# Performance work log

Measured on AMD Instinct MI355X. Metric: run time of the kernel, lower is better.

The kernel has to match this reference:

```python
import jax, jax.numpy as jnp
import numpy as np

N_NODES = 50000
N_EDGES = 500000
F_IN = 16
F_OUT = 16
F_EDGE = 16
HIDDEN = 64


def setup_inputs() -> dict:
    key = jax.random.key(0)
    ks = jax.random.split(key, 9)
    return {
        "x": jax.random.normal(ks[0], (N_NODES, F_IN), dtype=jnp.float32),
        "edge_feat": jax.random.normal(ks[1], (N_EDGES, F_EDGE), dtype=jnp.float32),
        "src": jax.random.randint(ks[2], (N_EDGES,), 0, N_NODES, dtype=jnp.int32),
        "dst": jax.random.randint(ks[3], (N_EDGES,), 0, N_NODES, dtype=jnp.int32),
        "W1": jax.random.normal(ks[4], (F_EDGE, HIDDEN), dtype=jnp.float32) * 0.1,
        "b1": jax.random.normal(ks[5], (HIDDEN,), dtype=jnp.float32) * 0.1,
        "W2": jax.random.normal(ks[6], (HIDDEN, F_IN * F_OUT), dtype=jnp.float32) * 0.1,
        "b2": jax.random.normal(ks[7], (F_IN * F_OUT,), dtype=jnp.float32) * 0.1,
        "bias": jax.random.normal(ks[8], (F_OUT,), dtype=jnp.float32) * 0.1,
    }


def reference(x, edge_feat, src, dst, W1, b1, W2, b2, bias):
    # WeightNet: per-edge MLP producing a [F_IN, F_OUT] weight matrix per edge
    h = jax.nn.relu(edge_feat @ W1 + b1)                 # [E, HIDDEN]
    W = (h @ W2 + b2).reshape(-1, F_IN, F_OUT)           # [E, F_IN, F_OUT]
    # message: bmm(src_h[E,1,in], W[E,in,out]) -> [E, F_OUT]
    msg = jnp.einsum('ei,eio->eo', x[src], W)
    # scatter-mean reduce over destination nodes
    msum = jax.ops.segment_sum(msg, dst, num_segments=N_NODES)
    cnt = jax.ops.segment_sum(jnp.ones((msg.shape[0],), dtype=msg.dtype), dst,
                              num_segments=N_NODES)
    mean = msum / jnp.maximum(cnt, 1.0)[:, None]
    # DGL update_all only updates nodes that receive messages; zero in-degree
    # nodes keep their input 'h' (valid since F_IN == F_OUT)
    out = jnp.where((cnt > 0)[:, None], mean, x)
    return out + bias[None, :]                           # [N, F_OUT]
```

## Files before the change

kernel.cpp:

```cpp
#include <hip/hip_runtime.h>

#define NN 50000
#define NE 500000
#define FIN 16
#define FOUT 16
#define HID 64
#define TROW 1040
#define NPW 16

typedef unsigned int  uint;
typedef unsigned short ushort;

__device__ __forceinline__ ushort f2bf(float f) {
    uint u = __float_as_uint(f);
    u += 0x7fffu + ((u >> 16) & 1u);
    return (ushort)(u >> 16);
}
__device__ __forceinline__ float bflo(uint u) { return __uint_as_float(u << 16); }
__device__ __forceinline__ float bfhi(uint u) { return __uint_as_float(u & 0xffff0000u); }


__global__ __launch_bounds__(256) void w2r_prep(
    const float* __restrict__ W2, const float* __restrict__ b2,
    float* __restrict__ W2R)
{
    const int t = blockIdx.x * blockDim.x + threadIdx.x;
    if (t >= 65 * 256) return;
    const int j = t >> 8;
    const int col = t & 255;
    const int i = col >> 4, o = col & 15;
    const float v = (j < 64) ? W2[j * 256 + col] : b2[col];
    W2R[j * 256 + o * 16 + i] = v;
}

__global__ __launch_bounds__(256) void count_both(
    const int* __restrict__ src, const int* __restrict__ dst,
    int* __restrict__ deg_s, int* __restrict__ pos_s, int* __restrict__ deg_d)
{
    const int e = blockIdx.x * blockDim.x + threadIdx.x;
    if (e >= NE) return;
    pos_s[e] = atomicAdd(deg_s + src[e], 1);
    atomicAdd(deg_d + dst[e], 1);
}

__global__ __launch_bounds__(1024) void dgc_scan2(
    const int* __restrict__ degA, int* __restrict__ offA,
    const int* __restrict__ degB, int* __restrict__ offB)
{
    const int* __restrict__ deg = blockIdx.x ? degB : degA;
    int* __restrict__ offs      = blockIdx.x ? offB : offA;
    __shared__ int wsum[16];
    const int tid = threadIdx.x;
    const int lane = tid & 63;
    const int wid = tid >> 6;
    int carry = 0;
    for (int base = 0; base < NN; base += 1024) {
        const int idx = base + tid;
        const int v = (idx < NN) ? deg[idx] : 0;
        int s = v;
        #pragma unroll
        for (int d = 1; d < 64; d <<= 1) {
            int t = __shfl_up(s, d, 64);
            if (lane >= d) s += t;
        }
        if (lane == 63) wsum[wid] = s;
        __syncthreads();
        if (wid == 0 && lane < 16) {
            int w = wsum[lane];
            #pragma unroll
            for (int d = 1; d < 16; d <<= 1) {
                int t = __shfl_up(w, d, 64);
                if (lane >= d) w += t;
            }
            wsum[lane] = w;
        }
        __syncthreads();
        const int wpre = (wid == 0) ? 0 : wsum[wid - 1];
        if (idx < NN) offs[idx] = carry + wpre + (s - v);
        carry += wsum[15];
        __syncthreads();
    }
    if (tid == 0) offs[NN] = carry;
}

__global__ __launch_bounds__(256) void scatter_src(
    const int* __restrict__ src, const int* __restrict__ pos_s,
    const int* __restrict__ offs_s, int* __restrict__ eidx_s)
{
    const int e = blockIdx.x * blockDim.x + threadIdx.x;
    if (e >= NE) return;
    eidx_s[offs_s[src[e]] + pos_s[e]] = e;
}

__global__ __launch_bounds__(256) void tprep4(
    const float* __restrict__ x, const float* __restrict__ W2R,
    ushort* __restrict__ T)
{
    __shared__ ushort w2b[65 * 288];
    const int tid = threadIdx.x;
    for (int g = tid; g < 65 * 256; g += 256) {
        const int j = g >> 8, col = g & 255;
        const int oo = col >> 4, ii = col & 15;
        w2b[j * 288 + oo * 18 + ii] = f2bf(W2R[g]);
    }
    __syncthreads();

    const int w = tid >> 6, lane = tid & 63;
    const int j4 = lane >> 4, o = lane & 15;
    const int nbase = (blockIdx.x * 4 + w) * NPW;

    for (int t = 0; t < NPW; ++t) {
        const int n = nbase + t;
        if (n >= NN) break;

        float xr[16];
        {
            const float4* p = reinterpret_cast<const float4*>(x) + (size_t)n * 4;
            float4 a = p[0], b = p[1], c = p[2], d = p[3];
            xr[0]=a.x; xr[1]=a.y; xr[2]=a.z;  xr[3]=a.w;
            xr[4]=b.x; xr[5]=b.y; xr[6]=b.z;  xr[7]=b.w;
            xr[8]=c.x; xr[9]=c.y; xr[10]=c.z; xr[11]=c.w;
            xr[12]=d.x; xr[13]=d.y; xr[14]=d.z; xr[15]=d.w;
        }

        ushort* tw = T + (size_t)n * TROW;
        #pragma unroll
        for (int k = 0; k < 17; ++k) {
            const int j = j4 + (k << 2);
            if (j < 65) {
                const uint* wu = reinterpret_cast<const uint*>(w2b + j * 288 + o * 18);
                float s = 0.f;
                #pragma unroll
                for (int q = 0; q < 8; ++q) {
                    const uint u = wu[q];
                    s = fmaf(xr[2 * q],     bflo(u), s);
                    s = fmaf(xr[2 * q + 1], bfhi(u), s);
                }
                tw[j * 16 + o] = f2bf(s);
            }
        }
    }
}

__global__ __launch_bounds__(256) void edge_msg2(
    const int* __restrict__ eidx_s, const int* __restrict__ src,
    const int* __restrict__ dst, const float* __restrict__ ef,
    const float* __restrict__ W1, const float* __restrict__ b1,
    const ushort* __restrict__ T, const int* __restrict__ offs_d,
    int* __restrict__ cur_d, float* __restrict__ msgbuf)
{
    const int k = blockIdx.x * blockDim.x + threadIdx.x;
    if (k >= NE) return;
    const int e = eidx_s[k];
    const int s = src[e];

    float efv[16];
    {
        const float4* p = reinterpret_cast<const float4*>(ef) + (size_t)e * 4;
        float4 a = p[0], b = p[1], c = p[2], d = p[3];
        efv[0]=a.x; efv[1]=a.y; efv[2]=a.z;  efv[3]=a.w;
        efv[4]=b.x; efv[5]=b.y; efv[6]=b.z;  efv[7]=b.w;
        efv[8]=c.x; efv[9]=c.y; efv[10]=c.z; efv[11]=c.w;
        efv[12]=d.x; efv[13]=d.y; efv[14]=d.z; efv[15]=d.w;
    }

    const ushort* tr = T + (size_t)s * TROW;
    float m[16];
    {
        uint4 a = *reinterpret_cast<const uint4*>(tr + 1024);
        uint4 b = *reinterpret_cast<const uint4*>(tr + 1032);
        m[0]=bflo(a.x);  m[1]=bfhi(a.x);  m[2]=bflo(a.y);  m[3]=bfhi(a.y);
        m[4]=bflo(a.z);  m[5]=bfhi(a.z);  m[6]=bflo(a.w);  m[7]=bfhi(a.w);
        m[8]=bflo(b.x);  m[9]=bfhi(b.x);  m[10]=bflo(b.y); m[11]=bfhi(b.y);
        m[12]=bflo(b.z); m[13]=bfhi(b.z); m[14]=bflo(b.w); m[15]=bfhi(b.w);
    }

    for (int j = 0; j < HID; ++j) {
        float hj = b1[j];
        #pragma unroll
        for (int i = 0; i < 16; ++i)
            hj = fmaf(efv[i], W1[i * HID + j], hj);
        hj = fmaxf(hj, 0.f);

        uint4 a = *reinterpret_cast<const uint4*>(tr + j * 16);
        uint4 b = *reinterpret_cast<const uint4*>(tr + j * 16 + 8);
        m[0]  = fmaf(hj, bflo(a.x), m[0]);  m[1]  = fmaf(hj, bfhi(a.x), m[1]);
        m[2]  = fmaf(hj, bflo(a.y), m[2]);  m[3]  = fmaf(hj, bfhi(a.y), m[3]);
        m[4]  = fmaf(hj, bflo(a.z), m[4]);  m[5]  = fmaf(hj, bfhi(a.z), m[5]);
        m[6]  = fmaf(hj, bflo(a.w), m[6]);  m[7]  = fmaf(hj, bfhi(a.w), m[7]);
        m[8]  = fmaf(hj, bflo(b.x), m[8]);  m[9]  = fmaf(hj, bfhi(b.x), m[9]);
        m[10] = fmaf(hj, bflo(b.y), m[10]); m[11] = fmaf(hj, bfhi(b.y), m[11]);
        m[12] = fmaf(hj, bflo(b.z), m[12]); m[13] = fmaf(hj, bfhi(b.z), m[13]);
        m[14] = fmaf(hj, bflo(b.w), m[14]); m[15] = fmaf(hj, bfhi(b.w), m[15]);
    }

    const int d = dst[e];
    const int slot = offs_d[d] + atomicAdd(cur_d + d, 1);
    float4* mr = reinterpret_cast<float4*>(msgbuf + (size_t)slot * 16);
    mr[0] = make_float4(m[0], m[1], m[2], m[3]);
    mr[1] = make_float4(m[4], m[5], m[6], m[7]);
    mr[2] = make_float4(m[8], m[9], m[10], m[11]);
    mr[3] = make_float4(m[12], m[13], m[14], m[15]);
}

__global__ __launch_bounds__(256) void gather_mean2(
    const float* __restrict__ msgbuf, const int* __restrict__ offs_d,
    const float* __restrict__ x, const float* __restrict__ bias,
    float* __restrict__ out)
{
    const int t = blockIdx.x * blockDim.x + threadIdx.x;
    if (t >= NN * FOUT) return;
    const int n = t >> 4;
    const int o = t & 15;
    const int beg = offs_d[n], end = offs_d[n + 1];
    float s = 0.f;
    for (int k = beg; k < end; ++k)
        s += msgbuf[(size_t)k * 16 + o];
    const int d = end - beg;
    const float v = (d > 0) ? (s / (float)d) : x[t];
    out[t] = v + bias[o];
}

__global__ __launch_bounds__(1024) void dgc_scan(
    const int* __restrict__ deg, int* __restrict__ offs, int n)
{
    __shared__ int wsum[16];
    const int tid = threadIdx.x;
    const int lane = tid & 63;
    const int wid = tid >> 6;
    int carry = 0;
    for (int base = 0; base < n; base += 1024) {
        const int idx = base + tid;
        const int v = (idx < n) ? deg[idx] : 0;
        int s = v;
        #pragma unroll
        for (int d = 1; d < 64; d <<= 1) {
            int t = __shfl_up(s, d, 64);
            if (lane >= d) s += t;
        }
        if (lane == 63) wsum[wid] = s;
        __syncthreads();
        if (wid == 0 && lane < 16) {
            int w = wsum[lane];
            #pragma unroll
            for (int d = 1; d < 16; d <<= 1) {
                int t = __shfl_up(w, d, 64);
                if (lane >= d) w += t;
            }
            wsum[lane] = w;
        }
        __syncthreads();
        const int wpre = (wid == 0) ? 0 : wsum[wid - 1];
        if (idx < n) offs[idx] = carry + wpre + (s - v);
        carry += wsum[15];
        __syncthreads();
    }
    if (tid == 0) offs[n] = carry;
}

__global__ __launch_bounds__(256) void dgc_edge_csr(
    const float* __restrict__ x, const float* __restrict__ ef,
    const int* __restrict__ src, const int* __restrict__ dst,
    const float* __restrict__ W1, const float* __restrict__ b1,
    const float* __restrict__ W2, const float* __restrict__ b2,
    float* __restrict__ msg, int* __restrict__ pos, int* __restrict__ deg)
{
    const int e = blockIdx.x * blockDim.x + threadIdx.x;
    if (e >= NE) return;
    float efv[16];
    {
        const float4* p = reinterpret_cast<const float4*>(ef) + (size_t)e * 4;
        float4 a = p[0], b = p[1], c = p[2], d = p[3];
        efv[0]=a.x; efv[1]=a.y; efv[2]=a.z;  efv[3]=a.w;
        efv[4]=b.x; efv[5]=b.y; efv[6]=b.z;  efv[7]=b.w;
        efv[8]=c.x; efv[9]=c.y; efv[10]=c.z; efv[11]=c.w;
        efv[12]=d.x; efv[13]=d.y; efv[14]=d.z; efv[15]=d.w;
    }
    const int s = src[e];
    float xs[16];
    {
        const float4* p = reinterpret_cast<const float4*>(x) + (size_t)s * 4;
        float4 a = p[0], b = p[1], c = p[2], d = p[3];
        xs[0]=a.x; xs[1]=a.y; xs[2]=a.z;  xs[3]=a.w;
        xs[4]=b.x; xs[5]=b.y; xs[6]=b.z;  xs[7]=b.w;
        xs[8]=c.x; xs[9]=c.y; xs[10]=c.z; xs[11]=c.w;
        xs[12]=d.x; xs[13]=d.y; xs[14]=d.z; xs[15]=d.w;
    }
    float m[16];
    #pragma unroll
    for (int o = 0; o < 16; ++o) m[o] = 0.f;
    #pragma unroll
    for (int i = 0; i < 16; ++i) {
        const float xi = xs[i];
        #pragma unroll
        for (int o = 0; o < 16; ++o) m[o] = fmaf(xi, b2[i * 16 + o], m[o]);
    }
    for (int j = 0; j < HID; ++j) {
        float hj = b1[j];
        #pragma unroll
        for (int i = 0; i < 16; ++i) hj = fmaf(efv[i], W1[i * HID + j], hj);
        hj = fmaxf(hj, 0.f);
        const float* __restrict__ w2r = W2 + (size_t)j * 256;
        float t[16];
        #pragma unroll
        for (int o = 0; o < 16; ++o) t[o] = 0.f;
        #pragma unroll
        for (int i = 0; i < 16; ++i) {
            const float xi = xs[i];
            #pragma unroll
            for (int o = 0; o < 16; ++o) t[o] = fmaf(xi, w2r[i * 16 + o], t[o]);
        }
        #pragma unroll
        for (int o = 0; o < 16; ++o) m[o] = fmaf(hj, t[o], m[o]);
    }
    float4* mr = reinterpret_cast<float4*>(msg + (size_t)e * 16);
    mr[0] = make_float4(m[0], m[1], m[2], m[3]);
    mr[1] = make_float4(m[4], m[5], m[6], m[7]);
    mr[2] = make_float4(m[8], m[9], m[10], m[11]);
    mr[3] = make_float4(m[12], m[13], m[14], m[15]);
    pos[e] = atomicAdd(deg + dst[e], 1);
}

__global__ __launch_bounds__(256) void dgc_scatter(
    const int* __restrict__ dst, const int* __restrict__ pos,
    const int* __restrict__ offs, int* __restrict__ eidx)
{
    const int e = blockIdx.x * blockDim.x + threadIdx.x;
    if (e >= NE) return;
    eidx[offs[dst[e]] + pos[e]] = e;
}

__global__ __launch_bounds__(256) void dgc_gather(
    const float* __restrict__ msg, const int* __restrict__ offs,
    const int* __restrict__ eidx, const float* __restrict__ x,
    const float* __restrict__ bias, float* __restrict__ out)
{
    const int t = blockIdx.x * blockDim.x + threadIdx.x;
    if (t >= NN * FOUT) return;
    const int n = t >> 4;
    const int o = t & 15;
    const int beg = offs[n], end = offs[n + 1];
    float s = 0.f;
    for (int k = beg; k < end; ++k)
        s += msg[(size_t)eidx[k] * 16 + o];
    const int d = end - beg;
    const float v = (d > 0) ? (s / (float)d) : x[t];
    out[t] = v + bias[o];
}

extern "C" void kernel_launch(void* const* d_in, const int* in_sizes, int n_in,
                              void* d_out, int out_size, void* d_ws, size_t ws_size,
                              hipStream_t stream) {
    const float* x    = (const float*)d_in[0];
    const float* ef   = (const float*)d_in[1];
    const int*   src  = (const int*)d_in[2];
    const int*   dst  = (const int*)d_in[3];
    const float* W1   = (const float*)d_in[4];
    const float* b1   = (const float*)d_in[5];
    const float* W2   = (const float*)d_in[6];
    const float* b2   = (const float*)d_in[7];
    const float* bias = (const float*)d_in[8];
    float* out = (float*)d_out;

    ushort* T      = (ushort*)d_ws;
    float*  msgbuf = (float*)(T + (size_t)NN * TROW);
    float*  W2R    = msgbuf + (size_t)NE * 16;
    int*    deg_s  = (int*)(W2R + 65 * 256);
    int*    deg_d  = deg_s + NN;
    int*    cur_d  = deg_d + NN;
    int*    offs_s = cur_d + NN;
    int*    offs_d = offs_s + NN + 1;
    int*    pos_s  = offs_d + NN + 1;
    int*    eidx_s = pos_s + NE;
    const size_t needed =
        (size_t)NN * TROW * 2 +
        ((size_t)NE * 16 + 65 * 256) * 4 +
        ((size_t)3 * NN + 2 * (NN + 1) + (size_t)2 * NE) * 4;

    if (ws_size >= needed) {
        hipMemsetAsync(deg_s, 0, (size_t)3 * NN * sizeof(int), stream);
        w2r_prep<<<(65 * 256 + 255) / 256, 256, 0, stream>>>(W2, b2, W2R);
        count_both<<<(NE + 255) / 256, 256, 0, stream>>>(src, dst, deg_s, pos_s, deg_d);
        dgc_scan2<<<2, 1024, 0, stream>>>(deg_s, offs_s, deg_d, offs_d);
        scatter_src<<<(NE + 255) / 256, 256, 0, stream>>>(src, pos_s, offs_s, eidx_s);
        tprep4<<<(NN + 4 * NPW - 1) / (4 * NPW), 256, 0, stream>>>(x, W2R, T);
        edge_msg2<<<(NE + 255) / 256, 256, 0, stream>>>(
            eidx_s, src, dst, ef, W1, b1, T, offs_d, cur_d, msgbuf);
        gather_mean2<<<(NN * FOUT + 255) / 256, 256, 0, stream>>>(
            msgbuf, offs_d, x, bias, out);
    } else {
        float* msg  = (float*)d_ws;
        int*   deg  = (int*)(msg + (size_t)NE * 16);
        int*   offs = deg + NN;
        int*   pos  = offs + NN + 1;
        int*   eidx = pos + NE;
        hipMemsetAsync(deg, 0, (size_t)NN * sizeof(int), stream);
        dgc_edge_csr<<<(NE + 255) / 256, 256, 0, stream>>>(
            x, ef, src, dst, W1, b1, W2, b2, msg, pos, deg);
        dgc_scan<<<1, 1024, 0, stream>>>(deg, offs, NN);
        dgc_scatter<<<(NE + 255) / 256, 256, 0, stream>>>(dst, pos, offs, eidx);
        dgc_gather<<<(NN * FOUT + 255) / 256, 256, 0, stream>>>(
            msg, offs, eidx, x, bias, out);
    }
}
```

Before: 259.9 us.

## Keep W2 slices in registers for T prep and process two edges per thread

The per-node T-table kernel now keeps each thread's W2R slices in fp32 registers and uses a grid-stride loop over nodes, one node per block iteration. This replaces the shared-memory bf16 staging of the weights and the per-block conversion cost. The edge message kernel now handles two consecutive sorted edges per thread, sharing W1 loads across both and exposing more independent loads and FMAs. The cost is higher register pressure, which may reduce occupancy. Skipping the bf16 rounding of the weights also changes numerics slightly.

```diff
diff --git a/kernel.cpp b/kernel.cpp
--- a/kernel.cpp
+++ b/kernel.cpp
@@ -6,7 +6,6 @@
 #define FOUT 16
 #define HID 64
 #define TROW 1040
-#define NPW 16
 
 typedef unsigned int  uint;
 typedef unsigned short ushort;
@@ -92,27 +91,37 @@
     eidx_s[offs_s[src[e]] + pos_s[e]] = e;
 }
 
-__global__ __launch_bounds__(256) void tprep4(
+__global__ __launch_bounds__(256) void tprep5(
     const float* __restrict__ x, const float* __restrict__ W2R,
     ushort* __restrict__ T)
 {
-    __shared__ ushort w2b[65 * 288];
     const int tid = threadIdx.x;
-    for (int g = tid; g < 65 * 256; g += 256) {
-        const int j = g >> 8, col = g & 255;
-        const int oo = col >> 4, ii = col & 15;
-        w2b[j * 288 + oo * 18 + ii] = f2bf(W2R[g]);
-    }
-    __syncthreads();
-
-    const int w = tid >> 6, lane = tid & 63;
-    const int j4 = lane >> 4, o = lane & 15;
-    const int nbase = (blockIdx.x * 4 + w) * NPW;
-
-    for (int t = 0; t < NPW; ++t) {
-        const int n = nbase + t;
-        if (n >= NN) break;
-
+    const int jt = tid >> 4, o = tid & 15;
+
+    float w0[16], w1[16], w2[16], w3[16];
+    {
+        const float4* p0 = reinterpret_cast<const float4*>(W2R + (jt     ) * 256 + o * 16);
+        const float4* p1 = reinterpret_cast<const float4*>(W2R + (jt + 16) * 256 + o * 16);
+        const float4* p2 = reinterpret_cast<const float4*>(W2R + (jt + 32) * 256 + o * 16);
+        const float4* p3 = reinterpret_cast<const float4*>(W2R + (jt + 48) * 256 + o * 16);
+        #pragma unroll
+        for (int q = 0; q < 4; ++q) {
+            float4 a = p0[q]; w0[4*q]=a.x; w0[4*q+1]=a.y; w0[4*q+2]=a.z; w0[4*q+3]=a.w;
+            float4 b = p1[q]; w1[4*q]=b.x; w1[4*q+1]=b.y; w1[4*q+2]=b.z; w1[4*q+3]=b.w;
+            float4 c = p2[q]; w2[4*q]=c.x; w2[4*q+1]=c.y; w2[4*q+2]=c.z; w2[4*q+3]=c.w;
+            float4 d = p3[q]; w3[4*q]=d.x; w3[4*q+1]=d.y; w3[4*q+2]=d.z; w3[4*q+3]=d.w;
+        }
+    }
+    float wb[16];
+    if (jt == 0) {
+        const float4* pb = reinterpret_cast<const float4*>(W2R + 64 * 256 + o * 16);
+        #pragma unroll
+        for (int q = 0; q < 4; ++q) {
+            float4 a = pb[q]; wb[4*q]=a.x; wb[4*q+1]=a.y; wb[4*q+2]=a.z; wb[4*q+3]=a.w;
+        }
+    }
+
+    for (int n = blockIdx.x; n < NN; n += gridDim.x) {
         float xr[16];
         {
             const float4* p = reinterpret_cast<const float4*>(x) + (size_t)n * 4;
@@ -122,85 +131,134 @@
             xr[8]=c.x; xr[9]=c.y; xr[10]=c.z; xr[11]=c.w;
             xr[12]=d.x; xr[13]=d.y; xr[14]=d.z; xr[15]=d.w;
         }
-
         ushort* tw = T + (size_t)n * TROW;
-        #pragma unroll
-        for (int k = 0; k < 17; ++k) {
-            const int j = j4 + (k << 2);
-            if (j < 65) {
-                const uint* wu = reinterpret_cast<const uint*>(w2b + j * 288 + o * 18);
-                float s = 0.f;
-                #pragma unroll
-                for (int q = 0; q < 8; ++q) {
-                    const uint u = wu[q];
-                    s = fmaf(xr[2 * q],     bflo(u), s);
-                    s = fmaf(xr[2 * q + 1], bfhi(u), s);
-                }
-                tw[j * 16 + o] = f2bf(s);
-            }
-        }
-    }
-}
-
-__global__ __launch_bounds__(256) void edge_msg2(
+
+        float s0 = xr[0]*w0[0], s1 = xr[0]*w1[0], s2 = xr[0]*w2[0], s3 = xr[0]*w3[0];
+        #pragma unroll
+        for (int i = 1; i < 16; ++i) {
+            s0 = fmaf(xr[i], w0[i], s0);
+            s1 = fmaf(xr[i], w1[i], s1);
+            s2 = fmaf(xr[i], w2[i], s2);
+            s3 = fmaf(xr[i], w3[i], s3);
+        }
+        tw[tid]       = f2bf(s0);
+        tw[tid + 256] = f2bf(s1);
+        tw[tid + 512] = f2bf(s2);
+        tw[tid + 768] = f2bf(s3);
+        if (jt == 0) {
+            float sb = xr[0]*wb[0];
+            #pragma unroll
+            for (int i = 1; i < 16; ++i) sb = fmaf(xr[i], wb[i], sb);
+            tw[1024 + o] = f2bf(sb);
+        }
+    }
+}
+
+__global__ __launch_bounds__(256) void edge_msg3(
     const int* __restrict__ eidx_s, const int* __restrict__ src,
     const int* __restrict__ dst, const float* __restrict__ ef,
     const float* __restrict__ W1, const float* __restrict__ b1,
     const ushort* __restrict__ T, const int* __restrict__ offs_d,
     int* __restrict__ cur_d, float* __restrict__ msgbuf)
 {
-    const int k = blockIdx.x * blockDim.x + threadIdx.x;
-    if (k >= NE) return;
-    const int e = eidx_s[k];
-    const int s = src[e];
-
-    float efv[16];
-    {
-        const float4* p = reinterpret_cast<const float4*>(ef) + (size_t)e * 4;
+    const int k0 = (blockIdx.x * blockDim.x + threadIdx.x) * 2;
+    if (k0 >= NE) return;
+    const bool two = (k0 + 1 < NE);
+    const int k1 = two ? (k0 + 1) : k0;
+
+    const int e0 = eidx_s[k0], e1 = eidx_s[k1];
+    const int s0 = src[e0],    s1 = src[e1];
+
+    float ea[16], eb[16];
+    {
+        const float4* p = reinterpret_cast<const float4*>(ef) + (size_t)e0 * 4;
         float4 a = p[0], b = p[1], c = p[2], d = p[3];
-        efv[0]=a.x; efv[1]=a.y; efv[2]=a.z;  efv[3]=a.w;
-        efv[4]=b.x; efv[5]=b.y; efv[6]=b.z;  efv[7]=b.w;
-        efv[8]=c.x; efv[9]=c.y; efv[10]=c.z; efv[11]=c.w;
-        efv[12]=d.x; efv[13]=d.y; efv[14]=d.z; efv[15]=d.w;
-    }
-
-    const ushort* tr = T + (size_t)s * TROW;
-    float m[16];
-    {
-        uint4 a = *reinterpret_cast<const uint4*>(tr + 1024);
-        uint4 b = *reinterpret_cast<const uint4*>(tr + 1032);
-        m[0]=bflo(a.x);  m[1]=bfhi(a.x);  m[2]=bflo(a.y);  m[3]=bfhi(a.y);
-        m[4]=bflo(a.z);  m[5]=bfhi(a.z);  m[6]=bflo(a.w);  m[7]=bfhi(a.w);
-        m[8]=bflo(b.x);  m[9]=bfhi(b.x);  m[10]=bflo(b.y); m[11]=bfhi(b.y);
-        m[12]=bflo(b.z); m[13]=bfhi(b.z); m[14]=bflo(b.w); m[15]=bfhi(b.w);
+        ea[0]=a.x; ea[1]=a.y; ea[2]=a.z;  ea[3]=a.w;
+        ea[4]=b.x; ea[5]=b.y; ea[6]=b.z;  ea[7]=b.w;
+        ea[8]=c.x; ea[9]=c.y; ea[10]=c.z; ea[11]=c.w;
+        ea[12]=d.x; ea[13]=d.y; ea[14]=d.z; ea[15]=d.w;
+    }
+    {
+        const float4* p = reinterpret_cast<const float4*>(ef) + (size_t)e1 * 4;
+        float4 a = p[0], b = p[1], c = p[2], d = p[3];
+        eb[0]=a.x; eb[1]=a.y; eb[2]=a.z;  eb[3]=a.w;
+        eb[4]=b.x; eb[5]=b.y; eb[6]=b.z;  eb[7]=b.w;
+        eb[8]=c.x; eb[9]=c.y; eb[10]=c.z; eb[11]=c.w;
+        eb[12]=d.x; eb[13]=d.y; eb[14]=d.z; eb[15]=d.w;
+    }
+
+    const ushort* tr0 = T + (size_t)s0 * TROW;
+    const ushort* tr1 = T + (size_t)s1 * TROW;
+
+    float m0[16], m1[16];
+    {
+        uint4 a = *reinterpret_cast<const uint4*>(tr0 + 1024);
+        uint4 b = *reinterpret_cast<const uint4*>(tr0 + 1032);
+        m0[0]=bflo(a.x);  m0[1]=bfhi(a.x);  m0[2]=bflo(a.y);  m0[3]=bfhi(a.y);
+        m0[4]=bflo(a.z);  m0[5]=bfhi(a.z);  m0[6]=bflo(a.w);  m0[7]=bfhi(a.w);
+        m0[8]=bflo(b.x);  m0[9]=bfhi(b.x);  m0[10]=bflo(b.y); m0[11]=bfhi(b.y);
+        m0[12]=bflo(b.z); m0[13]=bfhi(b.z); m0[14]=bflo(b.w); m0[15]=bfhi(b.w);
+    }
+    {
+        uint4 a = *reinterpret_cast<const uint4*>(tr1 + 1024);
+        uint4 b = *reinterpret_cast<const uint4*>(tr1 + 1032);
+        m1[0]=bflo(a.x);  m1[1]=bfhi(a.x);  m1[2]=bflo(a.y);  m1[3]=bfhi(a.y);
+        m1[4]=bflo(a.z);  m1[5]=bfhi(a.z);  m1[6]=bflo(a.w);  m1[7]=bfhi(a.w);
+        m1[8]=bflo(b.x);  m1[9]=bfhi(b.x);  m1[10]=bflo(b.y); m1[11]=bfhi(b.y);
+        m1[12]=bflo(b.z); m1[13]=bfhi(b.z); m1[14]=bflo(b.w); m1[15]=bfhi(b.w);
     }
 
     for (int j = 0; j < HID; ++j) {
-        float hj = b1[j];
-        #pragma unroll
-        for (int i = 0; i < 16; ++i)
-            hj = fmaf(efv[i], W1[i * HID + j], hj);
-        hj = fmaxf(hj, 0.f);
-
-        uint4 a = *reinterpret_cast<const uint4*>(tr + j * 16);
-        uint4 b = *reinterpret_cast<const uint4*>(tr + j * 16 + 8);
-        m[0]  = fmaf(hj, bflo(a.x), m[0]);  m[1]  = fmaf(hj, bfhi(a.x), m[1]);
-        m[2]  = fmaf(hj, bflo(a.y), m[2]);  m[3]  = fmaf(hj, bfhi(a.y), m[3]);
-        m[4]  = fmaf(hj, bflo(a.z), m[4]);  m[5]  = fmaf(hj, bfhi(a.z), m[5]);
-        m[6]  = fmaf(hj, bflo(a.w), m[6]);  m[7]  = fmaf(hj, bfhi(a.w), m[7]);
-        m[8]  = fmaf(hj, bflo(b.x), m[8]);  m[9]  = fmaf(hj, bfhi(b.x), m[9]);
-        m[10] = fmaf(hj, bflo(b.y), m[10]); m[11] = fmaf(hj, bfhi(b.y), m[11]);
-        m[12] = fmaf(hj, bflo(b.z), m[12]); m[13] = fmaf(hj, bfhi(b.z), m[13]);
-        m[14] = fmaf(hj, bflo(b.w), m[14]); m[15] = fmaf(hj, bfhi(b.w), m[15]);
-    }
-
-    const int d = dst[e];
-    const int slot = offs_d[d] + atomicAdd(cur_d + d, 1);
-    float4* mr = reinterpret_cast<float4*>(msgbuf + (size_t)slot * 16);
-    mr[0] = make_float4(m[0], m[1], m[2], m[3]);
-    mr[1] = make_float4(m[4], m[5], m[6], m[7]);
-    mr[2] = make_float4(m[8], m[9], m[10], m[11]);
-    mr[3] = make_float4(m[12], m[13], m[14], m[15]);
+        float h0 = b1[j], h1 = h0;
+        #pragma unroll
+        for (int i = 0; i < 16; ++i) {
+            const float w = W1[i * HID + j];
+            h0 = fmaf(ea[i], w, h0);
+            h1 = fmaf(eb[i], w, h1);
+        }
+        h0 = fmaxf(h0, 0.f);
+        h1 = fmaxf(h1, 0.f);
+
+        uint4 a0 = *reinterpret_cast<const uint4*>(tr0 + j * 16);
+        uint4 b0 = *reinterpret_cast<const uint4*>(tr0 + j * 16 + 8);
+        uint4 a1 = *reinterpret_cast<const uint4*>(tr1 + j * 16);
+        uint4 b1v = *reinterpret_cast<const uint4*>(tr1 + j * 16 + 8);
+        m0[0]  = fmaf(h0, bflo(a0.x), m0[0]);  m0[1]  = fmaf(h0, bfhi(a0.x), m0[1]);
+        m0[2]  = fmaf(h0, bflo(a0.y), m0[2]);  m0[3]  = fmaf(h0, bfhi(a0.y), m0[3]);
+        m0[4]  = fmaf(h0, bflo(a0.z), m0[4]);  m0[5]  = fmaf(h0, bfhi(a0.z), m0[5]);
+        m0[6]  = fmaf(h0, bflo(a0.w), m0[6]);  m0[7]  = fmaf(h0, bfhi(a0.w), m0[7]);
+        m0[8]  = fmaf(h0, bflo(b0.x), m0[8]);  m0[9]  = fmaf(h0, bfhi(b0.x), m0[9]);
+        m0[10] = fmaf(h0, bflo(b0.y), m0[10]); m0[11] = fmaf(h0, bfhi(b0.y), m0[11]);
+        m0[12] = fmaf(h0, bflo(b0.z), m0[12]); m0[13] = fmaf(h0, bfhi(b0.z), m0[13]);
+        m0[14] = fmaf(h0, bflo(b0.w), m0[14]); m0[15] = fmaf(h0, bfhi(b0.w), m0[15]);
+        m1[0]  = fmaf(h1, bflo(a1.x), m1[0]);  m1[1]  = fmaf(h1, bfhi(a1.x), m1[1]);
+        m1[2]  = fmaf(h1, bflo(a1.y), m1[2]);  m1[3]  = fmaf(h1, bfhi(a1.y), m1[3]);
+        m1[4]  = fmaf(h1, bflo(a1.z), m1[4]);  m1[5]  = fmaf(h1, bfhi(a1.z), m1[5]);
+        m1[6]  = fmaf(h1, bflo(a1.w), m1[6]);  m1[7]  = fmaf(h1, bfhi(a1.w), m1[7]);
+        m1[8]  = fmaf(h1, bflo(b1v.x), m1[8]);  m1[9]  = fmaf(h1, bfhi(b1v.x), m1[9]);
+        m1[10] = fmaf(h1, bflo(b1v.y), m1[10]); m1[11] = fmaf(h1, bfhi(b1v.y), m1[11]);
+        m1[12] = fmaf(h1, bflo(b1v.z), m1[12]); m1[13] = fmaf(h1, bfhi(b1v.z), m1[13]);
+        m1[14] = fmaf(h1, bflo(b1v.w), m1[14]); m1[15] = fmaf(h1, bfhi(b1v.w), m1[15]);
+    }
+
+    {
+        const int d = dst[e0];
+        const int slot = offs_d[d] + atomicAdd(cur_d + d, 1);
+        float4* mr = reinterpret_cast<float4*>(msgbuf + (size_t)slot * 16);
+        mr[0] = make_float4(m0[0], m0[1], m0[2], m0[3]);
+        mr[1] = make_float4(m0[4], m0[5], m0[6], m0[7]);
+        mr[2] = make_float4(m0[8], m0[9], m0[10], m0[11]);
+        mr[3] = make_float4(m0[12], m0[13], m0[14], m0[15]);
+    }
+    if (two) {
+        const int d = dst[e1];
+        const int slot = offs_d[d] + atomicAdd(cur_d + d, 1);
+        float4* mr = reinterpret_cast<float4*>(msgbuf + (size_t)slot * 16);
+        mr[0] = make_float4(m1[0], m1[1], m1[2], m1[3]);
+        mr[1] = make_float4(m1[4], m1[5], m1[6], m1[7]);
+        mr[2] = make_float4(m1[8], m1[9], m1[10], m1[11]);
+        mr[3] = make_float4(m1[12], m1[13], m1[14], m1[15]);
+    }
 }
 
 __global__ __launch_bounds__(256) void gather_mean2(
@@ -383,8 +441,8 @@
         count_both<<<(NE + 255) / 256, 256, 0, stream>>>(src, dst, deg_s, pos_s, deg_d);
         dgc_scan2<<<2, 1024, 0, stream>>>(deg_s, offs_s, deg_d, offs_d);
         scatter_src<<<(NE + 255) / 256, 256, 0, stream>>>(src, pos_s, offs_s, eidx_s);
-        tprep4<<<(NN + 4 * NPW - 1) / (4 * NPW), 256, 0, stream>>>(x, W2R, T);
-        edge_msg2<<<(NE + 255) / 256, 256, 0, stream>>>(
+        tprep5<<<2048, 256, 0, stream>>>(x, W2R, T);
+        edge_msg3<<<(NE / 2 + 255) / 256, 256, 0, stream>>>(
             eidx_s, src, dst, ef, W1, b1, T, offs_d, cur_d, msgbuf);
         gather_mean2<<<(NN * FOUT + 255) / 256, 256, 0, stream>>>(
             msgbuf, offs_d, x, bias, out);
```

Result: faster. 233.2 us (-10.3%).

## Register-resident W2 in T precompute, transposed W1 chunks, atomic-free dst slots

Applied to the files above, without the earlier changes.

The per-node T precompute now keeps its W2 slice in fp32 registers and runs a grid-stride loop with one node per block iteration, instead of staging bf16 weights in shared memory. The edge kernel reads a transposed W1 and computes hidden units in chunks of 16, giving a contiguous weight access pattern and more instruction-level parallelism. The destination slot comes from a position recorded during the count pass, so the per-edge atomic on a cursor array is gone, at the cost of an extra NE-sized int buffer. Register pressure rises in both kernels.

```diff
diff --git a/kernel.cpp b/kernel.cpp
--- a/kernel.cpp
+++ b/kernel.cpp
@@ -6,7 +6,6 @@
 #define FOUT 16
 #define HID 64
 #define TROW 1040
-#define NPW 16
 
 typedef unsigned int  uint;
 typedef unsigned short ushort;
@@ -22,9 +21,14 @@
 
 __global__ __launch_bounds__(256) void w2r_prep(
     const float* __restrict__ W2, const float* __restrict__ b2,
-    float* __restrict__ W2R)
+    const float* __restrict__ W1, float* __restrict__ W2R,
+    float* __restrict__ W1T)
 {
     const int t = blockIdx.x * blockDim.x + threadIdx.x;
+    if (t < 64 * 16) {
+        const int j = t >> 4, i = t & 15;
+        W1T[t] = W1[i * HID + j];
+    }
     if (t >= 65 * 256) return;
     const int j = t >> 8;
     const int col = t & 255;
@@ -35,12 +39,13 @@
 
 __global__ __launch_bounds__(256) void count_both(
     const int* __restrict__ src, const int* __restrict__ dst,
-    int* __restrict__ deg_s, int* __restrict__ pos_s, int* __restrict__ deg_d)
+    int* __restrict__ deg_s, int* __restrict__ pos_s,
+    int* __restrict__ deg_d, int* __restrict__ pos_d)
 {
     const int e = blockIdx.x * blockDim.x + threadIdx.x;
     if (e >= NE) return;
     pos_s[e] = atomicAdd(deg_s + src[e], 1);
-    atomicAdd(deg_d + dst[e], 1);
+    pos_d[e] = atomicAdd(deg_d + dst[e], 1);
 }
 
 __global__ __launch_bounds__(1024) void dgc_scan2(
@@ -92,27 +97,37 @@
     eidx_s[offs_s[src[e]] + pos_s[e]] = e;
 }
 
-__global__ __launch_bounds__(256) void tprep4(
+__global__ __launch_bounds__(256) void tprep5(
     const float* __restrict__ x, const float* __restrict__ W2R,
     ushort* __restrict__ T)
 {
-    __shared__ ushort w2b[65 * 288];
     const int tid = threadIdx.x;
-    for (int g = tid; g < 65 * 256; g += 256) {
-        const int j = g >> 8, col = g & 255;
-        const int oo = col >> 4, ii = col & 15;
-        w2b[j * 288 + oo * 18 + ii] = f2bf(W2R[g]);
-    }
-    __syncthreads();
-
-    const int w = tid >> 6, lane = tid & 63;
-    const int j4 = lane >> 4, o = lane & 15;
-    const int nbase = (blockIdx.x * 4 + w) * NPW;
-
-    for (int t = 0; t < NPW; ++t) {
-        const int n = nbase + t;
-        if (n >= NN) break;
-
+    const int jt = tid >> 4, o = tid & 15;
+
+    float w0[16], w1[16], w2[16], w3[16];
+    {
+        const float4* p0 = reinterpret_cast<const float4*>(W2R + (jt     ) * 256 + o * 16);
+        const float4* p1 = reinterpret_cast<const float4*>(W2R + (jt + 16) * 256 + o * 16);
+        const float4* p2 = reinterpret_cast<const float4*>(W2R + (jt + 32) * 256 + o * 16);
+        const float4* p3 = reinterpret_cast<const float4*>(W2R + (jt + 48) * 256 + o * 16);
+        #pragma unroll
+        for (int q = 0; q < 4; ++q) {
+            float4 a = p0[q]; w0[4*q]=a.x; w0[4*q+1]=a.y; w0[4*q+2]=a.z; w0[4*q+3]=a.w;
+            float4 b = p1[q]; w1[4*q]=b.x; w1[4*q+1]=b.y; w1[4*q+2]=b.z; w1[4*q+3]=b.w;
+            float4 c = p2[q]; w2[4*q]=c.x; w2[4*q+1]=c.y; w2[4*q+2]=c.z; w2[4*q+3]=c.w;
+            float4 d = p3[q]; w3[4*q]=d.x; w3[4*q+1]=d.y; w3[4*q+2]=d.z; w3[4*q+3]=d.w;
+        }
+    }
+    float wb[16];
+    if (jt == 0) {
+        const float4* pb = reinterpret_cast<const float4*>(W2R + 64 * 256 + o * 16);
+        #pragma unroll
+        for (int q = 0; q < 4; ++q) {
+            float4 a = pb[q]; wb[4*q]=a.x; wb[4*q+1]=a.y; wb[4*q+2]=a.z; wb[4*q+3]=a.w;
+        }
+    }
+
+    for (int n = blockIdx.x; n < NN; n += gridDim.x) {
         float xr[16];
         {
             const float4* p = reinterpret_cast<const float4*>(x) + (size_t)n * 4;
@@ -122,32 +137,35 @@
             xr[8]=c.x; xr[9]=c.y; xr[10]=c.z; xr[11]=c.w;
             xr[12]=d.x; xr[13]=d.y; xr[14]=d.z; xr[15]=d.w;
         }
-
         ushort* tw = T + (size_t)n * TROW;
-        #pragma unroll
-        for (int k = 0; k < 17; ++k) {
-            const int j = j4 + (k << 2);
-            if (j < 65) {
-                const uint* wu = reinterpret_cast<const uint*>(w2b + j * 288 + o * 18);
-                float s = 0.f;
-                #pragma unroll
-                for (int q = 0; q < 8; ++q) {
-                    const uint u = wu[q];
-                    s = fmaf(xr[2 * q],     bflo(u), s);
-                    s = fmaf(xr[2 * q + 1], bfhi(u), s);
-                }
-                tw[j * 16 + o] = f2bf(s);
-            }
-        }
-    }
-}
-
-__global__ __launch_bounds__(256) void edge_msg2(
+
+        float s0 = xr[0]*w0[0], s1 = xr[0]*w1[0], s2 = xr[0]*w2[0], s3 = xr[0]*w3[0];
+        #pragma unroll
+        for (int i = 1; i < 16; ++i) {
+            s0 = fmaf(xr[i], w0[i], s0);
+            s1 = fmaf(xr[i], w1[i], s1);
+            s2 = fmaf(xr[i], w2[i], s2);
+            s3 = fmaf(xr[i], w3[i], s3);
+        }
+        tw[tid]       = f2bf(s0);
+        tw[tid + 256] = f2bf(s1);
+        tw[tid + 512] = f2bf(s2);
+        tw[tid + 768] = f2bf(s3);
+        if (jt == 0) {
+            float sb = xr[0]*wb[0];
+            #pragma unroll
+            for (int i = 1; i < 16; ++i) sb = fmaf(xr[i], wb[i], sb);
+            tw[1024 + o] = f2bf(sb);
+        }
+    }
+}
+
+__global__ __launch_bounds__(256) void edge_msg4(
     const int* __restrict__ eidx_s, const int* __restrict__ src,
     const int* __restrict__ dst, const float* __restrict__ ef,
-    const float* __restrict__ W1, const float* __restrict__ b1,
+    const float* __restrict__ W1T, const float* __restrict__ b1,
     const ushort* __restrict__ T, const int* __restrict__ offs_d,
-    int* __restrict__ cur_d, float* __restrict__ msgbuf)
+    const int* __restrict__ pos_d, float* __restrict__ msgbuf)
 {
     const int k = blockIdx.x * blockDim.x + threadIdx.x;
     if (k >= NE) return;
@@ -175,27 +193,39 @@
         m[12]=bflo(b.z); m[13]=bfhi(b.z); m[14]=bflo(b.w); m[15]=bfhi(b.w);
     }
 
-    for (int j = 0; j < HID; ++j) {
-        float hj = b1[j];
-        #pragma unroll
-        for (int i = 0; i < 16; ++i)
-            hj = fmaf(efv[i], W1[i * HID + j], hj);
-        hj = fmaxf(hj, 0.f);
-
-        uint4 a = *reinterpret_cast<const uint4*>(tr + j * 16);
-        uint4 b = *reinterpret_cast<const uint4*>(tr + j * 16 + 8);
-        m[0]  = fmaf(hj, bflo(a.x), m[0]);  m[1]  = fmaf(hj, bfhi(a.x), m[1]);
-        m[2]  = fmaf(hj, bflo(a.y), m[2]);  m[3]  = fmaf(hj, bfhi(a.y), m[3]);
-        m[4]  = fmaf(hj, bflo(a.z), m[4]);  m[5]  = fmaf(hj, bfhi(a.z), m[5]);
-        m[6]  = fmaf(hj, bflo(a.w), m[6]);  m[7]  = fmaf(hj, bfhi(a.w), m[7]);
-        m[8]  = fmaf(hj, bflo(b.x), m[8]);  m[9]  = fmaf(hj, bfhi(b.x), m[9]);
-        m[10] = fmaf(hj, bflo(b.y), m[10]); m[11] = fmaf(hj, bfhi(b.y), m[11]);
-        m[12] = fmaf(hj, bflo(b.z), m[12]); m[13] = fmaf(hj, bfhi(b.z), m[13]);
-        m[14] = fmaf(hj, bflo(b.w), m[14]); m[15] = fmaf(hj, bfhi(b.w), m[15]);
+    for (int jc = 0; jc < 4; ++jc) {
+        const float*  wc = W1T + jc * 256;
+        const float*  bc = b1 + jc * 16;
+        const ushort* tc = tr + jc * 256;
+
+        float hh[16];
+        #pragma unroll
+        for (int jj = 0; jj < 16; ++jj) {
+            float hj = bc[jj];
+            #pragma unroll
+            for (int i = 0; i < 16; ++i)
+                hj = fmaf(efv[i], wc[jj * 16 + i], hj);
+            hh[jj] = fmaxf(hj, 0.f);
+        }
+
+        #pragma unroll
+        for (int jj = 0; jj < 16; ++jj) {
+            const float h = hh[jj];
+            uint4 a = *reinterpret_cast<const uint4*>(tc + jj * 16);
+            uint4 b = *reinterpret_cast<const uint4*>(tc + jj * 16 + 8);
+            m[0]  = fmaf(h, bflo(a.x), m[0]);  m[1]  = fmaf(h, bfhi(a.x), m[1]);
+            m[2]  = fmaf(h, bflo(a.y), m[2]);  m[3]  = fmaf(h, bfhi(a.y), m[3]);
+            m[4]  = fmaf(h, bflo(a.z), m[4]);  m[5]  = fmaf(h, bfhi(a.z), m[5]);
+            m[6]  = fmaf(h, bflo(a.w), m[6]);  m[7]  = fmaf(h, bfhi(a.w), m[7]);
+            m[8]  = fmaf(h, bflo(b.x), m[8]);  m[9]  = fmaf(h, bfhi(b.x), m[9]);
+            m[10] = fmaf(h, bflo(b.y), m[10]); m[11] = fmaf(h, bfhi(b.y), m[11]);
+            m[12] = fmaf(h, bflo(b.z), m[12]); m[13] = fmaf(h, bfhi(b.z), m[13]);
+            m[14] = fmaf(h, bflo(b.w), m[14]); m[15] = fmaf(h, bfhi(b.w), m[15]);
+        }
     }
 
     const int d = dst[e];
-    const int slot = offs_d[d] + atomicAdd(cur_d + d, 1);
+    const int slot = offs_d[d] + pos_d[e];
     float4* mr = reinterpret_cast<float4*>(msgbuf + (size_t)slot * 16);
     mr[0] = make_float4(m[0], m[1], m[2], m[3]);
     mr[1] = make_float4(m[4], m[5], m[6], m[7]);
@@ -365,27 +395,28 @@
     ushort* T      = (ushort*)d_ws;
     float*  msgbuf = (float*)(T + (size_t)NN * TROW);
     float*  W2R    = msgbuf + (size_t)NE * 16;
-    int*    deg_s  = (int*)(W2R + 65 * 256);
+    float*  W1T    = W2R + 65 * 256;
+    int*    deg_s  = (int*)(W1T + 64 * 16);
     int*    deg_d  = deg_s + NN;
-    int*    cur_d  = deg_d + NN;
-    int*    offs_s = cur_d + NN;
+    int*    offs_s = deg_d + NN;
     int*    offs_d = offs_s + NN + 1;
     int*    pos_s  = offs_d + NN + 1;
-    int*    eidx_s = pos_s + NE;
+    int*    pos_d  = pos_s + NE;
+    int*    eidx_s = pos_d + NE;
     const size_t needed =
         (size_t)NN * TROW * 2 +
-        ((size_t)NE * 16 + 65 * 256) * 4 +
-        ((size_t)3 * NN + 2 * (NN + 1) + (size_t)2 * NE) * 4;
+        ((size_t)NE * 16 + 65 * 256 + 64 * 16) * 4 +
+        ((size_t)2 * NN + 2 * (NN + 1) + (size_t)3 * NE) * 4;
 
     if (ws_size >= needed) {
-        hipMemsetAsync(deg_s, 0, (size_t)3 * NN * sizeof(int), stream);
-        w2r_prep<<<(65 * 256 + 255) / 256, 256, 0, stream>>>(W2, b2, W2R);
-        count_both<<<(NE + 255) / 256, 256, 0, stream>>>(src, dst, deg_s, pos_s, deg_d);
+        hipMemsetAsync(deg_s, 0, (size_t)2 * NN * sizeof(int), stream);
+        w2r_prep<<<(65 * 256 + 255) / 256, 256, 0, stream>>>(W2, b2, W1, W2R, W1T);
+        count_both<<<(NE + 255) / 256, 256, 0, stream>>>(src, dst, deg_s, pos_s, deg_d, pos_d);
         dgc_scan2<<<2, 1024, 0, stream>>>(deg_s, offs_s, deg_d, offs_d);
         scatter_src<<<(NE + 255) / 256, 256, 0, stream>>>(src, pos_s, offs_s, eidx_s);
-        tprep4<<<(NN + 4 * NPW - 1) / (4 * NPW), 256, 0, stream>>>(x, W2R, T);
-        edge_msg2<<<(NE + 255) / 256, 256, 0, stream>>>(
-            eidx_s, src, dst, ef, W1, b1, T, offs_d, cur_d, msgbuf);
+        tprep5<<<2048, 256, 0, stream>>>(x, W2R, T);
+        edge_msg4<<<(NE + 255) / 256, 256, 0, stream>>>(
+            eidx_s, src, dst, ef, W1T, b1, T, offs_d, pos_d, msgbuf);
         gather_mean2<<<(NN * FOUT + 255) / 256, 256, 0, stream>>>(
             msgbuf, offs_d, x, bias, out);
     } else {
```

Measured after the change: 263.1 us. No clear change (+1.2%).
